# Kernel tuning notes

Hardware: AMD Instinct MI355X
Metric: run time of the kernel (lower is better)

The kernel has to match this reference:

```python
import jax, jax.numpy as jnp
import numpy as np
from jax import lax

CIN, COUT, K_EXP, KSZ = 128, 256, 8, 3
HIDDEN = CIN // 4  # reduction=4
B, H, W = 32, 56, 56
TEMP = 1.0


def setup_inputs() -> dict:
    key = jax.random.key(0)
    ks = jax.random.split(key, 6)
    x = jax.random.normal(ks[0], (B, CIN, H, W), dtype=jnp.float32)
    weight_bank = jax.random.normal(ks[1], (K_EXP, COUT, CIN, KSZ, KSZ), dtype=jnp.float32) * 0.02
    fc1_w = jax.random.normal(ks[2], (HIDDEN, CIN), dtype=jnp.float32) * (1.0 / np.sqrt(CIN))
    fc1_b = jnp.zeros((HIDDEN,), dtype=jnp.float32)
    fc2_w = jax.random.normal(ks[3], (K_EXP, HIDDEN), dtype=jnp.float32) * (1.0 / np.sqrt(HIDDEN))
    fc2_b = jnp.zeros((K_EXP,), dtype=jnp.float32)
    return {"x": x, "weight_bank": weight_bank, "fc1_w": fc1_w, "fc1_b": fc1_b,
            "fc2_w": fc2_w, "fc2_b": fc2_b}


def reference(x, weight_bank, fc1_w, fc1_b, fc2_w, fc2_b):
    b, cin, h, w = x.shape
    # Routing: GAP -> fc1 -> relu -> fc2 -> softmax(/T)
    v = jnp.mean(x, axis=(2, 3))                       # (B, cin)
    hdd = jax.nn.relu(v @ fc1_w.T + fc1_b)             # (B, hidden)
    logits = hdd @ fc2_w.T + fc2_b                     # (B, K)
    a = jax.nn.softmax(logits / TEMP, axis=1)          # (B, K)
    # Per-sample dynamic weights: (B, cout, cin, k, k)
    Wdyn = jnp.einsum('bk,kocij->bocij', a, weight_bank)
    # Batched per-sample conv via grouped convolution:
    # x -> (1, B*cin, H, W), Wdyn -> (B*cout, cin, k, k), groups=B
    xg = x.reshape(1, b * cin, h, w)
    wg = Wdyn.reshape(b * weight_bank.shape[1], cin, KSZ, KSZ)
    y = lax.conv_general_dilated(
        xg, wg,
        window_strides=(1, 1),
        padding=[(1, 1), (1, 1)],
        feature_group_count=b,
        dimension_numbers=('NCHW', 'OIHW', 'NCHW'),
    )
    return y.reshape(b, weight_bank.shape[1], y.shape[2], y.shape[3])
```

## Files before the change

### kernel.cpp

```cpp
#include <hip/hip_runtime.h>


#define CIN    128
#define COUT   256
#define KEXP   8
#define HIDDEN 32
#define B_     32
#define H_     56
#define W_     56
#define HW     3136
#define HP     58
#define WP     58
#define KK     1152

typedef float  v4f  __attribute__((ext_vector_type(4)));
typedef __bf16 v8bf __attribute__((ext_vector_type(8)));

__device__ __forceinline__ unsigned short f2bf(float x) {
  unsigned int u = __float_as_uint(x);
  u += 0x7fff + ((u >> 16) & 1);
  return (unsigned short)(u >> 16);
}

__device__ __forceinline__ void gl_lds16(const void* g, void* lds) {
  __builtin_amdgcn_global_load_lds(
      (__attribute__((address_space(1))) void*)(unsigned long long)(g),
      (__attribute__((address_space(3))) void*)(lds),
      16, 0, 0);
}

__global__ __launch_bounds__(256) void k_xpose(const float* __restrict__ x,
                                               unsigned short* __restrict__ xpt,
                                               float* __restrict__ gpart) {
  const int h = blockIdx.x, b = blockIdx.y, tid = threadIdx.x;
  __shared__ float tf[56 * 129];
  __shared__ float gp[256];
  const float4* xr4 = (const float4*)x + (size_t)b * CIN * 784;

#pragma unroll
  for (int it = 0; it < 7; ++it) {
    int idx = it * 256 + tid;
    int c  = idx / 14;
    int wq = idx - c * 14;
    float4 q = xr4[(size_t)c * 784 + h * 14 + wq];
    int w0 = wq * 4;
    tf[(w0 + 0) * 129 + c] = q.x;
    tf[(w0 + 1) * 129 + c] = q.y;
    tf[(w0 + 2) * 129 + c] = q.z;
    tf[(w0 + 3) * 129 + c] = q.w;
  }
  __syncthreads();

  {
    int c = tid & 127, half = tid >> 7;
    float s = 0.f;
#pragma unroll
    for (int w = half * 28; w < half * 28 + 28; ++w) s += tf[w * 129 + c];
    gp[tid] = s;
  }

#pragma unroll
  for (int it = 0; it < 7; ++it) {
    int idx = it * 256 + tid;
    int w  = idx >> 5;
    int c4 = (idx & 31) << 2;
    ushort4 o;
    o.x = f2bf(tf[w * 129 + c4 + 0]);
    o.y = f2bf(tf[w * 129 + c4 + 1]);
    o.z = f2bf(tf[w * 129 + c4 + 2]);
    o.w = f2bf(tf[w * 129 + c4 + 3]);
    *(ushort4*)(xpt + ((size_t)(b * HP + (h + 1)) * WP + (w + 1)) * CIN + c4) = o;
  }

  if (tid < 128) {
    size_t rb = (size_t)(b * HP + (h + 1)) * WP * CIN;
    xpt[rb + tid] = 0;
    xpt[rb + 57 * CIN + tid] = 0;
  }
  if (h == 0 || h == 55) {
    int hr = (h == 0) ? 0 : 57;
    size_t rb = (size_t)(b * HP + hr) * WP * CIN;
    ushort4 z; z.x = z.y = z.z = z.w = 0;
    for (int i = tid; i < 1856; i += 256)
      *(ushort4*)(xpt + rb + i * 4) = z;
  }

  __syncthreads();
  if (tid < 128)
    gpart[((size_t)h * B_ + b) * CIN + tid] =
        (gp[tid] + gp[tid + 128]) * (1.0f / 3136.0f);
}

__global__ void k_mlp(const float* __restrict__ gpart, const float* __restrict__ fc1w,
                      const float* __restrict__ fc1b, const float* __restrict__ fc2w,
                      const float* __restrict__ fc2b, float* __restrict__ aout) {
  const int b = blockIdx.x, t = threadIdx.x;
  __shared__ float vS[CIN];
  __shared__ float hid[HIDDEN];
  __shared__ float lg[KEXP];
  {
    float s = 0.f;
    for (int h = 0; h < H_; ++h) s += gpart[((size_t)h * B_ + b) * CIN + t];
    vS[t] = s;
  }
  __syncthreads();
  if (t < HIDDEN) {
    float s = fc1b[t];
    const float* wr = fc1w + t * CIN;
    for (int c = 0; c < CIN; ++c) s += vS[c] * wr[c];
    hid[t] = fmaxf(s, 0.f);
  }
  __syncthreads();
  if (t < KEXP) {
    float s = fc2b[t];
    const float* wr = fc2w + t * HIDDEN;
    for (int j = 0; j < HIDDEN; ++j) s += hid[j] * wr[j];
    lg[t] = s;
  }
  __syncthreads();
  if (t == 0) {
    float m = lg[0];
    for (int k = 1; k < KEXP; ++k) m = fmaxf(m, lg[k]);
    float e[KEXP], den = 0.f;
    for (int k = 0; k < KEXP; ++k) { e[k] = expf(lg[k] - m); den += e[k]; }
    float inv = 1.0f / den;
    for (int k = 0; k < KEXP; ++k) aout[b * KEXP + k] = e[k] * inv;
  }
}

__global__ __launch_bounds__(512) void k_wdyn(const float* __restrict__ aout,
                                              const float* __restrict__ bank,
                                              unsigned short* __restrict__ wdyn) {
  const int cout = blockIdx.x, tid = threadIdx.x;
  __shared__ float4 bS4[KEXP * 288];
  __shared__ float aS[B_ * KEXP];

  for (int idx = tid; idx < KEXP * 288; idx += 512) {
    int k = idx / 288, r = idx - k * 288;
    bS4[idx] = ((const float4*)(bank + (size_t)(k * COUT + cout) * KK))[r];
  }
  if (tid < 256) aS[tid] = aout[tid];
  __syncthreads();

  const float* bS = (const float*)bS4;
  const int lane_kk = tid & 63;
  const int sg = tid >> 6;
  float areg[4][KEXP];
#pragma unroll
  for (int bi = 0; bi < 4; ++bi)
#pragma unroll
    for (int k = 0; k < KEXP; ++k) areg[bi][k] = aS[(sg * 4 + bi) * KEXP + k];

  for (int it = 0; it < 18; ++it) {
    int kk  = it * 64 + lane_kk;
    int khw = kk >> 7, cin = kk & 127;
    int e   = cin * 9 + khw;
    float vv[KEXP];
#pragma unroll
    for (int k = 0; k < KEXP; ++k) vv[k] = bS[k * KK + e];
#pragma unroll
    for (int bi = 0; bi < 4; ++bi) {
      float s = 0.f;
#pragma unroll
      for (int k = 0; k < KEXP; ++k) s += areg[bi][k] * vv[k];
      wdyn[(size_t)((sg * 4 + bi) * COUT + cout) * KK + kk] = f2bf(s);
    }
  }
}

__global__ __launch_bounds__(256) void k_conv(const unsigned short* __restrict__ wdyn,
                                              const unsigned short* __restrict__ xpt,
                                              float* __restrict__ out) {
  const int bx = blockIdx.x;
  const int b  = blockIdx.y;
  const int bm = bx & 1, ch = bx >> 1;
  const int p0 = ch * 128;
  const int tid = threadIdx.x;
  const int wv = tid >> 6, l = tid & 63;
  const int q = l >> 4, l15 = l & 15;
  const int mq = (wv & 1) * 64, nq = (wv >> 1) * 64;

  __shared__ __align__(16) unsigned short Ash[128 * 64];
  __shared__ __align__(16) unsigned short Bsh[128 * 64];

  const unsigned short* wb = wdyn + (size_t)(b * COUT + bm * 128) * KK;
  const unsigned short* xb = xpt + (size_t)b * HP * WP * CIN;

  int aoff[4], boff[4];
#pragma unroll
  for (int it = 0; it < 4; ++it) {
    int g = it * 256 + tid;
    int row = g >> 3;
    int c = (g & 7) ^ (row & 7);
    aoff[it] = row * KK + c * 8;
    int p = p0 + row;
    p = p > 3135 ? 3135 : p;
    int ph = p / 56, pw = p - ph * 56;
    boff[it] = (ph * WP + pw) * CIN + c * 8;
  }

  v4f acc[4][4];
#pragma unroll
  for (int i = 0; i < 4; ++i)
#pragma unroll
    for (int j = 0; j < 4; ++j)
#pragma unroll
      for (int rr = 0; rr < 4; ++rr) acc[i][j][rr] = 0.f;

#pragma unroll
  for (int t = 0; t < 18; ++t) {
    const int khw = t >> 1, cinb = (t & 1) << 6;
    const int kh = khw / 3, kw = khw - 3 * kh;
    const int bd = (kh * WP + kw) * CIN + cinb;
    const int ad = t * 64;
#pragma unroll
    for (int it = 0; it < 4; ++it)
      gl_lds16(wb + aoff[it] + ad, Ash + (it * 256 + wv * 64) * 8);
#pragma unroll
    for (int it = 0; it < 4; ++it)
      gl_lds16(xb + boff[it] + bd, Bsh + (it * 256 + wv * 64) * 8);
    __syncthreads();
#pragma unroll
    for (int ks = 0; ks < 2; ++ks) {
      v8bf af[4], bfr[4];
#pragma unroll
      for (int i = 0; i < 4; ++i) {
        int row = mq + 16 * i + l15;
        int phys = (q + 4 * ks) ^ (row & 7);
        af[i] = *(const v8bf*)(Ash + (row * 8 + phys) * 8);
      }
#pragma unroll
      for (int j = 0; j < 4; ++j) {
        int p = nq + 16 * j + l15;
        int phys = (q + 4 * ks) ^ (p & 7);
        bfr[j] = *(const v8bf*)(Bsh + (p * 8 + phys) * 8);
      }
#pragma unroll
      for (int i = 0; i < 4; ++i)
#pragma unroll
        for (int j = 0; j < 4; ++j)
          acc[i][j] = __builtin_amdgcn_mfma_f32_16x16x32_bf16(af[i], bfr[j],
                                                              acc[i][j], 0, 0, 0);
    }
    __syncthreads();
  }

#pragma unroll
  for (int j = 0; j < 4; ++j) {
    int p = p0 + nq + 16 * j + l15;
    if (p < HW) {
#pragma unroll
      for (int i = 0; i < 4; ++i) {
        int cout = bm * 128 + mq + 16 * i + 4 * q;
        float* op = out + (size_t)(b * COUT + cout) * HW + p;
#pragma unroll
        for (int rr = 0; rr < 4; ++rr) op[(size_t)rr * HW] = acc[i][j][rr];
      }
    }
  }
}

extern "C" void kernel_launch(void* const* d_in, const int* in_sizes, int n_in,
                              void* d_out, int out_size, void* d_ws, size_t ws_size,
                              hipStream_t stream) {
  const float* x    = (const float*)d_in[0];
  const float* bank = (const float*)d_in[1];
  const float* fc1w = (const float*)d_in[2];
  const float* fc1b = (const float*)d_in[3];
  const float* fc2w = (const float*)d_in[4];
  const float* fc2b = (const float*)d_in[5];
  float* out = (float*)d_out;

  char* ws = (char*)d_ws;
  float* gpart = (float*)(ws + 0);
  float* aout  = (float*)(ws + (1u << 20));
  unsigned short* wdyn = (unsigned short*)(ws + (2u << 20));
  unsigned short* xpt  = (unsigned short*)(ws + (2u << 20) + 18874368);

  k_xpose<<<dim3(H_, B_), 256, 0, stream>>>(x, xpt, gpart);
  k_mlp<<<dim3(B_), 128, 0, stream>>>(gpart, fc1w, fc1b, fc2w, fc2b, aout);
  k_wdyn<<<dim3(COUT), 512, 0, stream>>>(aout, bank, wdyn);
  k_conv<<<dim3(50, B_), 256, 0, stream>>>(wdyn, xpt, out);
}
```

Baseline: 240.5 us.

## Rewrite conv GEMM as 256x256 tile with double-buffered LDS pipeline

Replaces the 128x128-tile conv GEMM with a 256x256 tile per 512-thread block. It double-buffers A and B in 128KB of dynamic LDS, staging the next K-step with direct global-to-LDS loads interleaved between MFMA quadrants, and raises MFMA issue priority with setprio. Blocks are mapped so each XCD handles four samples for L2 locality. The aim is more reuse per LDS load and overlap of memory traffic with MFMA work. In exchange it uses more registers and LDS and needs many barriers, and the 416-block grid may leave some CUs idle.

```diff
diff --git a/kernel.cpp b/kernel.cpp
--- a/kernel.cpp
+++ b/kernel.cpp
@@ -168,93 +168,191 @@
   }
 }
 
-__global__ __launch_bounds__(256) void k_conv(const unsigned short* __restrict__ wdyn,
-                                              const unsigned short* __restrict__ xpt,
-                                              float* __restrict__ out) {
-  const int bx = blockIdx.x;
-  const int b  = blockIdx.y;
-  const int bm = bx & 1, ch = bx >> 1;
-  const int p0 = ch * 128;
+#define BARX()   asm volatile("s_barrier" ::: "memory")
+#define WAITV2() asm volatile("s_waitcnt vmcnt(2)" ::: "memory")
+#define WAITV0() asm volatile("s_waitcnt vmcnt(0)" ::: "memory")
+
+__device__ __forceinline__ void stage_a(const unsigned short* wb, unsigned short* Abuf,
+                                        int hf, int ad, const int (&aoffj)[2], int wv) {
+  const unsigned short* s = wb + hf * 128 * KK + ad;
+  unsigned short* d = Abuf + hf * 8192;
+  gl_lds16(s + aoffj[0], d + (wv * 64) * 8);
+  gl_lds16(s + aoffj[1], d + (512 + wv * 64) * 8);
+}
+
+__device__ __forceinline__ void stage_b(const unsigned short* xb, unsigned short* Bbuf,
+                                        int hf, int bd, const int (&boffj)[2][2], int wv) {
+  unsigned short* d = Bbuf + hf * 8192;
+  gl_lds16(xb + boffj[0][hf] + bd, d + (wv * 64) * 8);
+  gl_lds16(xb + boffj[1][hf] + bd, d + (512 + wv * 64) * 8);
+}
+
+template <int MH, int NH>
+__device__ __forceinline__ void load_quad(const unsigned short* Ab, const unsigned short* Bb,
+                                          int abase, int bbase, int pA, int pB,
+                                          v8bf (&af)[4][2], v8bf (&bv)[2][2]) {
+#pragma unroll
+  for (int mi = 0; mi < 4; ++mi) {
+    int r = abase + (MH * 4 + mi) * 1024;
+    af[mi][0] = *(const v8bf*)(Ab + r + pA);
+    af[mi][1] = *(const v8bf*)(Ab + r + pB);
+  }
+#pragma unroll
+  for (int ni = 0; ni < 2; ++ni) {
+    int r = bbase + (NH * 2 + ni) * 1024;
+    bv[ni][0] = *(const v8bf*)(Bb + r + pA);
+    bv[ni][1] = *(const v8bf*)(Bb + r + pB);
+  }
+}
+
+template <int MH, int NH>
+__device__ __forceinline__ void mfma_quad(v8bf (&af)[4][2], v8bf (&bv)[2][2],
+                                          v4f (&acc)[8][4]) {
+  __builtin_amdgcn_s_setprio(1);
+#pragma unroll
+  for (int mi = 0; mi < 4; ++mi)
+#pragma unroll
+    for (int ni = 0; ni < 2; ++ni) {
+      v4f& a = acc[MH * 4 + mi][NH * 2 + ni];
+      a = __builtin_amdgcn_mfma_f32_16x16x32_bf16(af[mi][0], bv[ni][0], a, 0, 0, 0);
+      a = __builtin_amdgcn_mfma_f32_16x16x32_bf16(af[mi][1], bv[ni][1], a, 0, 0, 0);
+    }
+  __builtin_amdgcn_s_setprio(0);
+}
+
+__global__ __launch_bounds__(512, 2) void k_conv256(const unsigned short* __restrict__ wdyn,
+                                                    const unsigned short* __restrict__ xpt,
+                                                    float* __restrict__ out) {
+  extern __shared__ unsigned short sh[];
+  unsigned short* As = sh;
+  unsigned short* Bs = sh + 32768;
+
+  const int id  = blockIdx.x;
+  const int xcd = id & 7, idx = id >> 3;
+  const int b   = xcd * 4 + idx / 13;
+  const int ch  = idx - (idx / 13) * 13;
+  const int p0  = ch << 8;
+
   const int tid = threadIdx.x;
   const int wv = tid >> 6, l = tid & 63;
-  const int q = l >> 4, l15 = l & 15;
-  const int mq = (wv & 1) * 64, nq = (wv >> 1) * 64;
-
-  __shared__ __align__(16) unsigned short Ash[128 * 64];
-  __shared__ __align__(16) unsigned short Bsh[128 * 64];
-
-  const unsigned short* wb = wdyn + (size_t)(b * COUT + bm * 128) * KK;
+  const int q4 = l >> 4, l15 = l & 15;
+  const int wr = wv >> 2, wc = wv & 3;
+
+  const unsigned short* wb = wdyn + (size_t)b * COUT * KK;
   const unsigned short* xb = xpt + (size_t)b * HP * WP * CIN;
 
-  int aoff[4], boff[4];
-#pragma unroll
-  for (int it = 0; it < 4; ++it) {
-    int g = it * 256 + tid;
-    int row = g >> 3;
-    int c = (g & 7) ^ (row & 7);
-    aoff[it] = row * KK + c * 8;
-    int p = p0 + row;
-    p = p > 3135 ? 3135 : p;
-    int ph = p / 56, pw = p - ph * 56;
-    boff[it] = (ph * WP + pw) * CIN + c * 8;
-  }
-
-  v4f acc[4][4];
-#pragma unroll
-  for (int i = 0; i < 4; ++i)
-#pragma unroll
-    for (int j = 0; j < 4; ++j)
-#pragma unroll
-      for (int rr = 0; rr < 4; ++rr) acc[i][j][rr] = 0.f;
-
-#pragma unroll
-  for (int t = 0; t < 18; ++t) {
-    const int khw = t >> 1, cinb = (t & 1) << 6;
-    const int kh = khw / 3, kw = khw - 3 * kh;
-    const int bd = (kh * WP + kw) * CIN + cinb;
-    const int ad = t * 64;
-#pragma unroll
-    for (int it = 0; it < 4; ++it)
-      gl_lds16(wb + aoff[it] + ad, Ash + (it * 256 + wv * 64) * 8);
-#pragma unroll
-    for (int it = 0; it < 4; ++it)
-      gl_lds16(xb + boff[it] + bd, Bsh + (it * 256 + wv * 64) * 8);
-    __syncthreads();
-#pragma unroll
-    for (int ks = 0; ks < 2; ++ks) {
-      v8bf af[4], bfr[4];
-#pragma unroll
-      for (int i = 0; i < 4; ++i) {
-        int row = mq + 16 * i + l15;
-        int phys = (q + 4 * ks) ^ (row & 7);
-        af[i] = *(const v8bf*)(Ash + (row * 8 + phys) * 8);
-      }
-#pragma unroll
-      for (int j = 0; j < 4; ++j) {
-        int p = nq + 16 * j + l15;
-        int phys = (q + 4 * ks) ^ (p & 7);
-        bfr[j] = *(const v8bf*)(Bsh + (p * 8 + phys) * 8);
-      }
-#pragma unroll
-      for (int i = 0; i < 4; ++i)
-#pragma unroll
-        for (int j = 0; j < 4; ++j)
-          acc[i][j] = __builtin_amdgcn_mfma_f32_16x16x32_bf16(af[i], bfr[j],
-                                                              acc[i][j], 0, 0, 0);
-    }
-    __syncthreads();
-  }
-
-#pragma unroll
-  for (int j = 0; j < 4; ++j) {
-    int p = p0 + nq + 16 * j + l15;
-    if (p < HW) {
-#pragma unroll
-      for (int i = 0; i < 4; ++i) {
-        int cout = bm * 128 + mq + 16 * i + 4 * q;
+  int aoffj[2];
+  int boffj[2][2];
+#pragma unroll
+  for (int j = 0; j < 2; ++j) {
+    int row0 = j * 64 + (tid >> 3);
+    int c = (tid & 7) ^ (row0 & 7);
+    aoffj[j] = row0 * KK + c * 8;
+#pragma unroll
+    for (int hf = 0; hf < 2; ++hf) {
+      int p = p0 + hf * 128 + row0;
+      p = p > 3135 ? 3135 : p;
+      int ph = p / 56, pw = p - ph * 56;
+      boffj[j][hf] = (ph * WP + pw) * CIN + c * 8;
+    }
+  }
+
+  const int abase = (wr * 128 + l15) * 64;
+  const int bbase = (wc * 64 + l15) * 64;
+  const int s7 = l15 & 7;
+  const int pA = (q4 ^ s7) * 8;
+  const int pB = ((q4 + 4) ^ s7) * 8;
+
+  v4f acc[8][4];
+#pragma unroll
+  for (int m = 0; m < 8; ++m)
+#pragma unroll
+    for (int n = 0; n < 4; ++n)
+#pragma unroll
+      for (int rr = 0; rr < 4; ++rr) acc[m][n][rr] = 0.f;
+
+  unsigned short* A0 = As;           unsigned short* B0 = Bs;
+  unsigned short* A1 = As + 16384;   unsigned short* B1 = Bs + 16384;
+
+  stage_a(wb, A0, 0, 0, aoffj, wv);
+  stage_a(wb, A0, 1, 0, aoffj, wv);
+  stage_b(xb, B0, 0, 0, boffj, wv);
+  stage_b(xb, B0, 1, 0, boffj, wv);
+  WAITV0();
+  BARX();
+
+  v8bf af[4][2], bv[2][2];
+  int kh = 0, kw = 0;
+  for (int i = 0; i < 9; ++i) {
+    int kw2 = kw + 1, kh2 = kh;
+    if (kw2 == 3) { kw2 = 0; kh2 = kh + 1; }
+    const int adO = (2 * i + 1) * 64;
+    const int adN = (2 * i + 2) * 64;
+    const int bdO = (kh * WP + kw) * CIN + 64;
+    const int bdN = (kh2 * WP + kw2) * CIN;
+    const bool lastI = (i == 8);
+
+    stage_a(wb, A1, 0, adO, aoffj, wv);
+    WAITV2();
+    BARX();
+    load_quad<0, 0>(A0, B0, abase, bbase, pA, pB, af, bv);
+    mfma_quad<0, 0>(af, bv, acc);
+    BARX();
+    load_quad<0, 1>(A0, B0, abase, bbase, pA, pB, af, bv);
+    stage_a(wb, A1, 1, adO, aoffj, wv);
+    BARX();
+    mfma_quad<0, 1>(af, bv, acc);
+    BARX();
+    load_quad<1, 0>(A0, B0, abase, bbase, pA, pB, af, bv);
+    stage_b(xb, B1, 0, bdO, boffj, wv);
+    BARX();
+    mfma_quad<1, 0>(af, bv, acc);
+    BARX();
+    load_quad<1, 1>(A0, B0, abase, bbase, pA, pB, af, bv);
+    stage_b(xb, B1, 1, bdO, boffj, wv);
+    BARX();
+    mfma_quad<1, 1>(af, bv, acc);
+    BARX();
+
+    if (!lastI) {
+      stage_a(wb, A0, 0, adN, aoffj, wv);
+      WAITV2();
+    } else {
+      WAITV0();
+    }
+    BARX();
+    load_quad<0, 0>(A1, B1, abase, bbase, pA, pB, af, bv);
+    mfma_quad<0, 0>(af, bv, acc);
+    BARX();
+    load_quad<0, 1>(A1, B1, abase, bbase, pA, pB, af, bv);
+    if (!lastI) stage_a(wb, A0, 1, adN, aoffj, wv);
+    BARX();
+    mfma_quad<0, 1>(af, bv, acc);
+    BARX();
+    load_quad<1, 0>(A1, B1, abase, bbase, pA, pB, af, bv);
+    if (!lastI) stage_b(xb, B0, 0, bdN, boffj, wv);
+    BARX();
+    mfma_quad<1, 0>(af, bv, acc);
+    BARX();
+    load_quad<1, 1>(A1, B1, abase, bbase, pA, pB, af, bv);
+    if (!lastI) stage_b(xb, B0, 1, bdN, boffj, wv);
+    BARX();
+    mfma_quad<1, 1>(af, bv, acc);
+    BARX();
+
+    kh = kh2; kw = kw2;
+  }
+
+#pragma unroll
+  for (int mf = 0; mf < 8; ++mf) {
+    int cout = wr * 128 + mf * 16 + 4 * q4;
+#pragma unroll
+    for (int nf = 0; nf < 4; ++nf) {
+      int p = p0 + wc * 64 + nf * 16 + l15;
+      if (p < HW) {
         float* op = out + (size_t)(b * COUT + cout) * HW + p;
 #pragma unroll
-        for (int rr = 0; rr < 4; ++rr) op[(size_t)rr * HW] = acc[i][j][rr];
+        for (int rr = 0; rr < 4; ++rr) op[(size_t)rr * HW] = acc[mf][nf][rr];
       }
     }
   }
@@ -277,8 +375,15 @@
   unsigned short* wdyn = (unsigned short*)(ws + (2u << 20));
   unsigned short* xpt  = (unsigned short*)(ws + (2u << 20) + 18874368);
 
+  static bool attr_done = false;
+  if (!attr_done) {
+    (void)hipFuncSetAttribute((const void*)k_conv256,
+                              hipFuncAttributeMaxDynamicSharedMemorySize, 131072);
+    attr_done = true;
+  }
+
   k_xpose<<<dim3(H_, B_), 256, 0, stream>>>(x, xpt, gpart);
   k_mlp<<<dim3(B_), 128, 0, stream>>>(gpart, fc1w, fc1b, fc2w, fc2b, aout);
   k_wdyn<<<dim3(COUT), 512, 0, stream>>>(aout, bank, wdyn);
-  k_conv<<<dim3(50, B_), 256, 0, stream>>>(wdyn, xpt, out);
-}
+  k_conv256<<<dim3(416), 512, 131072, stream>>>(wdyn, xpt, out);
+}
```

Measured after the change: 238.5 us. About the same (-0.8%).
